# Optimization experiments

Hardware: AMD Instinct MI355X
Metric: run time of the kernel (lower is better)

The kernel has to match this reference:

```python
import jax, jax.numpy as jnp
import numpy as np

N_NODES = 100000
N_EDGES = 400000   # number of hyperedges
N_INC = 1600000    # incidence pairs (node, hyperedge)
N_GRAPHS = 512
ATOM_DIM = 92
NODE_DIM = 64
H_DIM = 128
NUM_LAYERS = 3
BN_EPS = 1e-5


def setup_inputs() -> dict:
    key = jax.random.key(0)
    ks = jax.random.split(key, 10)
    x = jax.random.normal(ks[0], (N_NODES, ATOM_DIM), jnp.float32)
    node_idx = jax.random.randint(ks[1], (N_INC,), 0, N_NODES)
    edge_idx = jax.random.randint(ks[2], (N_INC,), 0, N_EDGES)
    batch = jnp.sort(jax.random.randint(ks[3], (N_NODES,), 0, N_GRAPHS))

    def lin(k, fan_in, shape):
        return jax.random.normal(k, shape, jnp.float32) / np.float32(np.sqrt(fan_in))

    W_emb = lin(ks[4], ATOM_DIM, (ATOM_DIM, NODE_DIM))
    b_emb = jnp.zeros((NODE_DIM,), jnp.float32)
    conv_W = lin(ks[5], NODE_DIM, (NUM_LAYERS, NODE_DIM, NODE_DIM))
    conv_b = jnp.zeros((NUM_LAYERS, NODE_DIM), jnp.float32)
    bn_gamma = jnp.ones((NUM_LAYERS, NODE_DIM), jnp.float32)
    bn_beta = jnp.zeros((NUM_LAYERS, NODE_DIM), jnp.float32)
    fc_W = lin(ks[6], NODE_DIM, (NODE_DIM, H_DIM))
    fc_b = jnp.zeros((H_DIM,), jnp.float32)
    fco_W = lin(ks[7], H_DIM, (H_DIM, 1))
    fco_b = jnp.zeros((1,), jnp.float32)
    return {
        "x": x, "W_emb": W_emb, "b_emb": b_emb,
        "conv_W": conv_W, "conv_b": conv_b,
        "bn_gamma": bn_gamma, "bn_beta": bn_beta,
        "fc_W": fc_W, "fc_b": fc_b, "fco_W": fco_W, "fco_b": fco_b,
        "node_idx": node_idx, "edge_idx": edge_idx, "batch": batch,
    }


def _hypergraph_conv(h, W, b, gamma, beta, node_idx, edge_idx):
    """PyG-style HypergraphConv: X' = D^-1 H B^-1 H^T (X Theta), then BN + softplus."""
    h = h @ W + b  # [N, F]
    ones = jnp.ones((N_INC,), h.dtype)
    deg_e = jax.ops.segment_sum(ones, edge_idx, num_segments=N_EDGES)  # |e| per hyperedge
    Binv = jnp.where(deg_e > 0, 1.0 / deg_e, 0.0)
    # node -> hyperedge: mean of member node features
    e_feat = jax.ops.segment_sum(h[node_idx], edge_idx, num_segments=N_EDGES) * Binv[:, None]
    deg_n = jax.ops.segment_sum(ones, node_idx, num_segments=N_NODES)  # node hyperedge-degree
    Dinv = jnp.where(deg_n > 0, 1.0 / deg_n, 0.0)
    # hyperedge -> node
    out = jax.ops.segment_sum(e_feat[edge_idx], node_idx, num_segments=N_NODES) * Dinv[:, None]
    # BatchNorm1d over node dimension (training-mode batch statistics, biased var)
    mean = out.mean(axis=0)
    var = jnp.mean(jnp.square(out - mean), axis=0)
    out = gamma * (out - mean) * jax.lax.rsqrt(var + BN_EPS) + beta
    return jax.nn.softplus(out)


def reference(x, W_emb, b_emb, conv_W, conv_b, bn_gamma, bn_beta,
              fc_W, fc_b, fco_W, fco_b, node_idx, edge_idx, batch):
    h = x @ W_emb + b_emb  # [N, node_dim]
    for l in range(NUM_LAYERS):
        h = _hypergraph_conv(h, conv_W[l], conv_b[l], bn_gamma[l], bn_beta[l],
                             node_idx, edge_idx)
    # scatter-mean pooling over graphs
    cnt = jax.ops.segment_sum(jnp.ones((N_NODES,), h.dtype), batch, num_segments=N_GRAPHS)
    pooled = jax.ops.segment_sum(h, batch, num_segments=N_GRAPHS) / jnp.maximum(cnt, 1.0)[:, None]
    g = jax.nn.softplus(pooled)
    g = jax.nn.softplus(g @ fc_W + fc_b)
    return g @ fco_W + fco_b  # [N_GRAPHS, 1]
```

## Files before the change

kernel.cpp:

```cpp
#include <hip/hip_runtime.h>
#include <hip/hip_fp16.h>
#include <math.h>

#define N_NODES   100000
#define N_EDGES   400000
#define N_INC     1600000
#define N_GRAPHS  512
#define ATOM_DIM  92
#define NODE_DIM  64
#define H_DIM     128
#define NUM_LAYERS 3
#define BN_EPS    1e-5f

#define NBUCK     391
#define PCHUNK    2048
#define NCHP      ((N_INC + PCHUNK - 1) / PCHUNK)
#define MM_BLOCKS 1568

struct alignas(8)  half4 { __half2 a, b; };
struct alignas(16) half8 { __half2 a, b, c, d; };
typedef __attribute__((ext_vector_type(8))) float float8;
typedef __attribute__((ext_vector_type(2))) float float2v;
typedef __attribute__((ext_vector_type(4))) float f32x4;
typedef _Float16 f16x8 __attribute__((ext_vector_type(8)));

__device__ __forceinline__ float softplus_f(float x) {
    return fmaxf(x, 0.f) + log1pf(expf(-fabsf(x)));
}

__device__ __forceinline__ float8 cvt8(half8 v) {
    float2 p0 = __half22float2(v.a), p1 = __half22float2(v.b);
    float2 p2 = __half22float2(v.c), p3 = __half22float2(v.d);
    float8 r;
    r[0] = p0.x; r[1] = p0.y; r[2] = p1.x; r[3] = p1.y;
    r[4] = p2.x; r[5] = p2.y; r[6] = p3.x; r[7] = p3.y;
    return r;
}
__device__ __forceinline__ half8 cvt16(float8 v) {
    half8 r;
    r.a = __floats2half2_rn(v[0], v[1]);
    r.b = __floats2half2_rn(v[2], v[3]);
    r.c = __floats2half2_rn(v[4], v[5]);
    r.d = __floats2half2_rn(v[6], v[7]);
    return r;
}

__device__ __forceinline__ float8 fp8x8_to_f32u(unsigned lo, unsigned hi) {
    float2v l0 = __builtin_amdgcn_cvt_pk_f32_fp8((int)lo, false);
    float2v h0 = __builtin_amdgcn_cvt_pk_f32_fp8((int)lo, true);
    float2v l1 = __builtin_amdgcn_cvt_pk_f32_fp8((int)hi, false);
    float2v h1 = __builtin_amdgcn_cvt_pk_f32_fp8((int)hi, true);
    float8 r;
    r[0] = l0.x; r[1] = l0.y; r[2] = h0.x; r[3] = h0.y;
    r[4] = l1.x; r[5] = l1.y; r[6] = h1.x; r[7] = h1.y;
    return r;
}
__device__ __forceinline__ float8 fp8x8_to_f32(uint2 v) {
    return fp8x8_to_f32u(v.x, v.y);
}
__device__ __forceinline__ uint2 f32_to_fp8x8(float8 v) {
    int a = 0, b = 0;
    a = __builtin_amdgcn_cvt_pk_fp8_f32(v[0], v[1], a, false);
    a = __builtin_amdgcn_cvt_pk_fp8_f32(v[2], v[3], a, true);
    b = __builtin_amdgcn_cvt_pk_fp8_f32(v[4], v[5], b, false);
    b = __builtin_amdgcn_cvt_pk_fp8_f32(v[6], v[7], b, true);
    uint2 r; r.x = (unsigned)a; r.y = (unsigned)b;
    return r;
}


__global__ void __launch_bounds__(256) embed_mfma(
        const float* __restrict__ x, const float* __restrict__ W,
        const float* __restrict__ bvec, uint2* __restrict__ h8) {
    __shared__ half8 so8[4][16][9];
    int tid = threadIdx.x;
    int w = tid >> 6, lane = tid & 63;
    int l15 = lane & 15, rg = lane >> 4;
    __half* so_h = (__half*)so8[w];

    f16x8 bf[4][3];
    #pragma unroll
    for (int c = 0; c < 4; ++c)
        #pragma unroll
        for (int kk = 0; kk < 3; ++kk)
            #pragma unroll
            for (int j = 0; j < 8; ++j) {
                int k = kk * 32 + rg * 8 + j;
                bf[c][kk][j] = (k < ATOM_DIM) ? (_Float16)W[k * 64 + c * 16 + l15]
                                              : (_Float16)0.f;
            }
    float bias[4];
    #pragma unroll
    for (int c = 0; c < 4; ++c) bias[c] = bvec[c * 16 + l15];

    int wave_global = blockIdx.x * 4 + w;
    for (int tile = wave_global; tile < N_NODES / 16; tile += MM_BLOCKS * 4) {
        int n0 = tile * 16;
        const float* xrow = x + (size_t)(n0 + l15) * ATOM_DIM;
        f16x8 af[3];
        #pragma unroll
        for (int kk = 0; kk < 3; ++kk) {
            int k0 = kk * 32 + rg * 8;
            if (k0 + 8 <= ATOM_DIM) {
                float4 v0 = *(const float4*)&xrow[k0];
                float4 v1 = *(const float4*)&xrow[k0 + 4];
                af[kk][0] = (_Float16)v0.x; af[kk][1] = (_Float16)v0.y;
                af[kk][2] = (_Float16)v0.z; af[kk][3] = (_Float16)v0.w;
                af[kk][4] = (_Float16)v1.x; af[kk][5] = (_Float16)v1.y;
                af[kk][6] = (_Float16)v1.z; af[kk][7] = (_Float16)v1.w;
            } else {
                float4 v0 = *(const float4*)&xrow[88];
                af[kk][0] = (_Float16)v0.x; af[kk][1] = (_Float16)v0.y;
                af[kk][2] = (_Float16)v0.z; af[kk][3] = (_Float16)v0.w;
                af[kk][4] = (_Float16)0.f;  af[kk][5] = (_Float16)0.f;
                af[kk][6] = (_Float16)0.f;  af[kk][7] = (_Float16)0.f;
            }
        }
        #pragma unroll
        for (int c = 0; c < 4; ++c) {
            f32x4 acc = {0.f, 0.f, 0.f, 0.f};
            acc = __builtin_amdgcn_mfma_f32_16x16x32_f16(af[0], bf[c][0], acc, 0, 0, 0);
            acc = __builtin_amdgcn_mfma_f32_16x16x32_f16(af[1], bf[c][1], acc, 0, 0, 0);
            acc = __builtin_amdgcn_mfma_f32_16x16x32_f16(af[2], bf[c][2], acc, 0, 0, 0);
            #pragma unroll
            for (int i = 0; i < 4; ++i)
                so_h[(rg * 4 + i) * 72 + c * 16 + l15] = __float2half_rn(acc[i] + bias[c]);
        }
        #pragma unroll
        for (int it = 0; it < 2; ++it) {
            int row = (lane >> 3) + it * 8;
            half8 v = *(half8*)&so_h[row * 72 + (lane & 7) * 8];
            h8[(size_t)(n0 + row) * 8 + (lane & 7)] = f32_to_fp8x8(cvt8(v));
        }
    }
}


__global__ void __launch_bounds__(256) part_hist_dual(
        const int* __restrict__ ekey, const int* __restrict__ nkey,
        int* __restrict__ histsE, int* __restrict__ histsN) {
    __shared__ int hE[NBUCK];
    __shared__ int hN[NBUCK];
    int tid = threadIdx.x;
    int base = blockIdx.x * PCHUNK;
    for (int i = tid; i < NBUCK; i += 256) { hE[i] = 0; hN[i] = 0; }
    __syncthreads();
    #pragma unroll
    for (int k = 0; k < 8; ++k) {
        int i = base + tid + k * 256;
        if (i < N_INC) {
            atomicAdd(&hE[ekey[i] >> 10], 1);
            atomicAdd(&hN[nkey[i] >> 8], 1);
        }
    }
    __syncthreads();
    for (int i = tid; i < NBUCK; i += 256) {
        histsE[(size_t)blockIdx.x * NBUCK + i] = hE[i];
        histsN[(size_t)blockIdx.x * NBUCK + i] = hN[i];
    }
}

__global__ void __launch_bounds__(256) col_scan_dual(
        int* __restrict__ histsE, int* __restrict__ histsN,
        int* __restrict__ colsumE, int* __restrict__ colsumN) {
    __shared__ int ws[256];
    int which = blockIdx.x >= NBUCK;
    int i = which ? (blockIdx.x - NBUCK) : blockIdx.x;
    int* hists = which ? histsN : histsE;
    int* colsum = which ? colsumN : colsumE;
    int tid = threadIdx.x;
    int v[4];
    int loc = 0;
    #pragma unroll
    for (int k = 0; k < 4; ++k) {
        int b = tid * 4 + k;
        v[k] = (b < NCHP) ? hists[(size_t)b * NBUCK + i] : 0;
        loc += v[k];
    }
    ws[tid] = loc;
    __syncthreads();
    for (int off = 1; off < 256; off <<= 1) {
        int t = (tid >= off) ? ws[tid - off] : 0;
        __syncthreads();
        ws[tid] += t;
        __syncthreads();
    }
    int run = ws[tid] - loc;
    if (tid == 255) colsum[i] = ws[255];
    #pragma unroll
    for (int k = 0; k < 4; ++k) {
        int b = tid * 4 + k;
        if (b < NCHP) hists[(size_t)b * NBUCK + i] = run;
        run += v[k];
    }
}

__global__ void bbase_scan_dual(const int* __restrict__ colsumE, const int* __restrict__ colsumN,
                                int* __restrict__ bbaseE, int* __restrict__ bbaseN) {
    __shared__ int sh[512];
    const int* colsum = blockIdx.x ? colsumN : colsumE;
    int* bbase = blockIdx.x ? bbaseN : bbaseE;
    int tid = threadIdx.x;
    int v = (tid < NBUCK) ? colsum[tid] : 0;
    sh[tid] = v;
    __syncthreads();
    for (int off = 1; off < 512; off <<= 1) {
        int t = (tid >= off) ? sh[tid - off] : 0;
        __syncthreads();
        sh[tid] += t;
        __syncthreads();
    }
    if (tid <= NBUCK)
        bbase[tid] = (tid == 0) ? 0 : sh[tid - 1];
}

__global__ void __launch_bounds__(256) part_scatter_dual(
        const int* __restrict__ ekey, const int* __restrict__ nkey,
        const int* __restrict__ histsE, const int* __restrict__ histsN,
        const int* __restrict__ bbaseE, const int* __restrict__ bbaseN,
        unsigned long long* __restrict__ stagingE,
        unsigned long long* __restrict__ stagingN) {
    __shared__ int curE[NBUCK];
    __shared__ int curN[NBUCK];
    int tid = threadIdx.x;
    int base = blockIdx.x * PCHUNK;
    int kE[8], kN[8];
    #pragma unroll
    for (int k = 0; k < 8; ++k) {
        int i = base + tid + k * 256;
        bool ok = (i < N_INC);
        kE[k] = ok ? ekey[i] : -1;
        kN[k] = ok ? nkey[i] : 0;
    }
    for (int i = tid; i < NBUCK; i += 256) {
        curE[i] = bbaseE[i] + histsE[(size_t)blockIdx.x * NBUCK + i];
        curN[i] = bbaseN[i] + histsN[(size_t)blockIdx.x * NBUCK + i];
    }
    __syncthreads();
    #pragma unroll
    for (int k = 0; k < 8; ++k) {
        if (kE[k] >= 0) {
            int pe = atomicAdd(&curE[kE[k] >> 10], 1);
            stagingE[pe] = ((unsigned long long)(unsigned)kE[k] << 32) | (unsigned)kN[k];
            int pn = atomicAdd(&curN[kN[k] >> 8], 1);
            stagingN[pn] = ((unsigned long long)(unsigned)kN[k] << 32) | (unsigned)kE[k];
        }
    }
}

template<int RANGE>
__global__ void bucket_finalize(const unsigned long long* __restrict__ staging,
                                const int* __restrict__ bbase,
                                int nIds, float* __restrict__ inv,
                                int* __restrict__ off, int* __restrict__ list) {
    __shared__ int hist[RANGE];
    __shared__ int wsum[256];
    const int PER = RANGE / 256;
    int b = blockIdx.x, tid = threadIdx.x;
    int s = bbase[b], t = bbase[b + 1];
    int id0 = b * RANGE;
    for (int i = tid; i < RANGE; i += 256) hist[i] = 0;
    __syncthreads();
    for (int j = s + tid; j < t; j += 256) {
        int key = (int)(staging[j] >> 32);
        atomicAdd(&hist[key - id0], 1);
    }
    __syncthreads();
    int base0 = tid * PER;
    int vals[PER];
    int local = 0;
    #pragma unroll
    for (int k = 0; k < PER; ++k) { vals[k] = hist[base0 + k]; local += vals[k]; }
    wsum[tid] = local;
    __syncthreads();
    for (int o = 1; o < 256; o <<= 1) {
        int tv = (tid >= o) ? wsum[tid - o] : 0;
        __syncthreads();
        wsum[tid] += tv;
        __syncthreads();
    }
    int run = wsum[tid] - local;
    #pragma unroll
    for (int k = 0; k < PER; ++k) {
        int id = id0 + base0 + k;
        int gpos = s + run;
        if (id < nIds) {
            off[id] = gpos;
            inv[id] = vals[k] > 0 ? 1.f / (float)vals[k] : 0.f;
        } else if (id == nIds) {
            off[nIds] = gpos;
        }
        hist[base0 + k] = gpos;
        run += vals[k];
    }
    __syncthreads();
    for (int j = s + tid; j < t; j += 256) {
        unsigned long long it = staging[j];
        int key = (int)(it >> 32);
        int pos = atomicAdd(&hist[key - id0], 1);
        list[pos] = (int)(it & 0xffffffffu);
    }
}


__global__ void __launch_bounds__(256) edge_agg(
        const int* __restrict__ eoff, const int* __restrict__ elist,
        const uint4* __restrict__ h16B, const float* __restrict__ binv,
        uint4* __restrict__ efeat16B) {
    int e = blockIdx.x * 64 + (threadIdx.x >> 2);
    if (e >= N_EDGES) return;
    int q = threadIdx.x & 3;
    int s = eoff[e], t = eoff[e + 1];
    float8 alo = (float8)0.f, ahi = (float8)0.f;
    float8 blo = (float8)0.f, bhi = (float8)0.f;
    int j = s;
    for (; j + 1 < t; j += 2) {
        int n0 = __ldg(&elist[j]), n1 = __ldg(&elist[j + 1]);
        uint4 v0 = __ldg(&h16B[(size_t)n0 * 4 + q]);
        uint4 v1 = __ldg(&h16B[(size_t)n1 * 4 + q]);
        alo += fp8x8_to_f32u(v0.x, v0.y); ahi += fp8x8_to_f32u(v0.z, v0.w);
        blo += fp8x8_to_f32u(v1.x, v1.y); bhi += fp8x8_to_f32u(v1.z, v1.w);
    }
    if (j < t) {
        uint4 v0 = __ldg(&h16B[(size_t)__ldg(&elist[j]) * 4 + q]);
        alo += fp8x8_to_f32u(v0.x, v0.y); ahi += fp8x8_to_f32u(v0.z, v0.w);
    }
    alo += blo; ahi += bhi;
    float bv = binv[e];
    alo *= bv; ahi *= bv;
    uint2 lo = f32_to_fp8x8(alo), hi = f32_to_fp8x8(ahi);
    uint4 st; st.x = lo.x; st.y = lo.y; st.z = hi.x; st.w = hi.y;
    efeat16B[(size_t)e * 4 + q] = st;
}

__global__ void __launch_bounds__(256) node_agg(
        const int* __restrict__ noff, const int* __restrict__ nlist,
        const uint4* __restrict__ efeat16B, const float* __restrict__ dinv,
        __half* __restrict__ agg16) {
    int n = blockIdx.x * 64 + (threadIdx.x >> 2);
    if (n >= N_NODES) return;
    int q = threadIdx.x & 3;
    int s = noff[n], t = noff[n + 1];
    float8 alo = (float8)0.f, ahi = (float8)0.f;
    float8 blo = (float8)0.f, bhi = (float8)0.f;
    int j = s;
    for (; j + 1 < t; j += 2) {
        int e0 = __ldg(&nlist[j]), e1 = __ldg(&nlist[j + 1]);
        uint4 v0 = __ldg(&efeat16B[(size_t)e0 * 4 + q]);
        uint4 v1 = __ldg(&efeat16B[(size_t)e1 * 4 + q]);
        alo += fp8x8_to_f32u(v0.x, v0.y); ahi += fp8x8_to_f32u(v0.z, v0.w);
        blo += fp8x8_to_f32u(v1.x, v1.y); bhi += fp8x8_to_f32u(v1.z, v1.w);
    }
    if (j < t) {
        uint4 v0 = __ldg(&efeat16B[(size_t)__ldg(&nlist[j]) * 4 + q]);
        alo += fp8x8_to_f32u(v0.x, v0.y); ahi += fp8x8_to_f32u(v0.z, v0.w);
    }
    alo += blo; ahi += bhi;
    float dv = dinv[n];
    alo *= dv; ahi *= dv;
    *(half8*)&agg16[(size_t)n * 64 + q * 16]     = cvt16(alo);
    *(half8*)&agg16[(size_t)n * 64 + q * 16 + 8] = cvt16(ahi);
}


__global__ void __launch_bounds__(256) gemm_bn_kernel(
        const __half* __restrict__ agg16, const float* __restrict__ dinv,
        const float* __restrict__ W, const float* __restrict__ bvec,
        __half* __restrict__ outr16, float* __restrict__ partials) {
    __shared__ half8 so8[4][16][9];
    __shared__ float sred[4][128];
    int tid = threadIdx.x;
    int w = tid >> 6, lane = tid & 63;
    int l15 = lane & 15, rg = lane >> 4;
    __half* so_h = (__half*)so8[w];

    f16x8 bf[4][2];
    #pragma unroll
    for (int c = 0; c < 4; ++c)
        #pragma unroll
        for (int kk = 0; kk < 2; ++kk)
            #pragma unroll
            for (int j = 0; j < 8; ++j) {
                int k = kk * 32 + rg * 8 + j;
                bf[c][kk][j] = (_Float16)W[k * 64 + c * 16 + l15];
            }
    float bias[4];
    #pragma unroll
    for (int c = 0; c < 4; ++c) bias[c] = bvec[c * 16 + l15];

    float sa[4] = {0.f, 0.f, 0.f, 0.f}, sb[4] = {0.f, 0.f, 0.f, 0.f};
    int wave_global = blockIdx.x * 4 + w;
    for (int tile = wave_global; tile < N_NODES / 16; tile += MM_BLOCKS * 4) {
        int n0 = tile * 16;
        f16x8 a0 = *(const f16x8*)&agg16[(size_t)(n0 + l15) * 64 + rg * 8];
        f16x8 a1 = *(const f16x8*)&agg16[(size_t)(n0 + l15) * 64 + 32 + rg * 8];
        float dv[4];
        #pragma unroll
        for (int i = 0; i < 4; ++i) dv[i] = dinv[n0 + rg * 4 + i];
        #pragma unroll
        for (int c = 0; c < 4; ++c) {
            f32x4 acc = {0.f, 0.f, 0.f, 0.f};
            acc = __builtin_amdgcn_mfma_f32_16x16x32_f16(a0, bf[c][0], acc, 0, 0, 0);
            acc = __builtin_amdgcn_mfma_f32_16x16x32_f16(a1, bf[c][1], acc, 0, 0, 0);
            #pragma unroll
            for (int i = 0; i < 4; ++i) {
                float vv = (dv[i] > 0.f) ? (acc[i] + bias[c]) : 0.f;
                sa[c] += vv; sb[c] += vv * vv;
                so_h[(rg * 4 + i) * 72 + c * 16 + l15] = __float2half_rn(vv);
            }
        }
        #pragma unroll
        for (int it = 0; it < 2; ++it) {
            int row = (lane >> 3) + it * 8;
            half8 v = *(half8*)&so_h[row * 72 + (lane & 7) * 8];
            *(half8*)&outr16[(size_t)(n0 + row) * 64 + (lane & 7) * 8] = v;
        }
    }
    #pragma unroll
    for (int c = 0; c < 4; ++c) {
        sa[c] += __shfl_xor(sa[c], 16); sa[c] += __shfl_xor(sa[c], 32);
        sb[c] += __shfl_xor(sb[c], 16); sb[c] += __shfl_xor(sb[c], 32);
    }
    if (rg == 0) {
        #pragma unroll
        for (int c = 0; c < 4; ++c) {
            sred[w][c * 16 + l15]      = sa[c];
            sred[w][64 + c * 16 + l15] = sb[c];
        }
    }
    __syncthreads();
    if (tid < 128) {
        float v = sred[0][tid] + sred[1][tid] + sred[2][tid] + sred[3][tid];
        partials[(size_t)blockIdx.x * 128 + tid] = v;
    }
}


__global__ void __launch_bounds__(256) reduce_bnfin(
        const float* __restrict__ partials, const float* __restrict__ gamma,
        const float* __restrict__ beta, float* __restrict__ scsh) {
    __shared__ float ra[256];
    __shared__ float rb[256];
    int f = blockIdx.x, tid = threadIdx.x;
    float a = 0.f, b = 0.f;
    for (int j = tid; j < MM_BLOCKS; j += 256) {
        a += partials[(size_t)j * 128 + f];
        b += partials[(size_t)j * 128 + 64 + f];
    }
    ra[tid] = a; rb[tid] = b;
    __syncthreads();
    for (int s = 128; s > 0; s >>= 1) {
        if (tid < s) { ra[tid] += ra[tid + s]; rb[tid] += rb[tid + s]; }
        __syncthreads();
    }
    if (tid == 0) {
        const float invN = 1.f / (float)N_NODES;
        float mean = ra[0] * invN;
        float var  = rb[0] * invN - mean * mean;
        var = fmaxf(var, 0.f);
        float sc = gamma[f] * rsqrtf(var + BN_EPS);
        scsh[f]      = sc;
        scsh[64 + f] = beta[f] - mean * sc;
    }
}


__global__ void apply_kernel(const half8* __restrict__ outr8, const float* __restrict__ scsh,
                             uint2* __restrict__ h8) {
    int gid = blockIdx.x * 256 + threadIdx.x;
    if (gid >= N_NODES * 8) return;
    int qq = gid & 7;
    float8 v = cvt8(outr8[gid]);
    float4 sc0 = ((const float4*)scsh)[qq * 2];
    float4 sc1 = ((const float4*)scsh)[qq * 2 + 1];
    float4 sh0 = ((const float4*)(scsh + 64))[qq * 2];
    float4 sh1 = ((const float4*)(scsh + 64))[qq * 2 + 1];
    float8 r;
    r[0] = softplus_f(fmaf(v[0], sc0.x, sh0.x));
    r[1] = softplus_f(fmaf(v[1], sc0.y, sh0.y));
    r[2] = softplus_f(fmaf(v[2], sc0.z, sh0.z));
    r[3] = softplus_f(fmaf(v[3], sc0.w, sh0.w));
    r[4] = softplus_f(fmaf(v[4], sc1.x, sh1.x));
    r[5] = softplus_f(fmaf(v[5], sc1.y, sh1.y));
    r[6] = softplus_f(fmaf(v[6], sc1.z, sh1.z));
    r[7] = softplus_f(fmaf(v[7], sc1.w, sh1.w));
    h8[gid] = f32_to_fp8x8(r);
}


__global__ void graph_bounds(const int* __restrict__ batch, int* __restrict__ goff) {
    int g = blockIdx.x * 256 + threadIdx.x;
    if (g > N_GRAPHS) return;
    int lo = 0, hi = N_NODES;
    while (lo < hi) {
        int mid = (lo + hi) >> 1;
        if (batch[mid] < g) lo = mid + 1; else hi = mid;
    }
    goff[g] = lo;
}

__global__ void pool_head_kernel(const uint2* __restrict__ h8, const int* __restrict__ goff,
                                 const float* __restrict__ fcW, const float* __restrict__ fcb,
                                 const float* __restrict__ fcoW, const float* __restrict__ fcob,
                                 float* __restrict__ out) {
    __shared__ float8 part[32][8];
    __shared__ float p[64];
    __shared__ float red[128];
    int g = blockIdx.x, tid = threadIdx.x;
    int s = goff[g], t = goff[g + 1];
    int r = tid >> 3, q = tid & 7;
    float8 acc = (float8)0.f;
    for (int n = s + r; n < t; n += 32)
        acc += fp8x8_to_f32(__ldg(&h8[(size_t)n * 8 + q]));
    part[r][q] = acc;
    __syncthreads();
    for (int st = 16; st >= 1; st >>= 1) {
        if (r < st) part[r][q] += part[r + st][q];
        __syncthreads();
    }
    if (tid < 8) {
        float c = fmaxf((float)(t - s), 1.f);
        float8 v = part[0][tid];
        #pragma unroll
        for (int jj = 0; jj < 8; ++jj)
            p[tid * 8 + jj] = softplus_f(v[jj] / c);
    }
    __syncthreads();
    if (tid < 128) {
        float a = fcb[tid];
        #pragma unroll
        for (int k = 0; k < 64; ++k)
            a = fmaf(p[k], fcW[k * H_DIM + tid], a);
        red[tid] = softplus_f(a) * fcoW[tid];
    }
    __syncthreads();
    for (int st = 64; st > 0; st >>= 1) {
        if (tid < st) red[tid] += red[tid + st];
        __syncthreads();
    }
    if (tid == 0) out[g] = red[0] + fcob[0];
}


extern "C" void kernel_launch(void* const* d_in, const int* in_sizes, int n_in,
                              void* d_out, int out_size, void* d_ws, size_t ws_size,
                              hipStream_t stream) {
    const float* x      = (const float*)d_in[0];
    const float* W_emb  = (const float*)d_in[1];
    const float* b_emb  = (const float*)d_in[2];
    const float* conv_W = (const float*)d_in[3];
    const float* conv_b = (const float*)d_in[4];
    const float* bn_g   = (const float*)d_in[5];
    const float* bn_b   = (const float*)d_in[6];
    const float* fc_W   = (const float*)d_in[7];
    const float* fc_b   = (const float*)d_in[8];
    const float* fco_W  = (const float*)d_in[9];
    const float* fco_b  = (const float*)d_in[10];
    const int* node_idx = (const int*)d_in[11];
    const int* edge_idx = (const int*)d_in[12];
    const int* batch    = (const int*)d_in[13];
    float* out = (float*)d_out;

    uint2*  h8      = (uint2*)d_ws;
    __half* outr16  = (__half*)(h8 + (size_t)N_NODES * 8);
    __half* agg16   = outr16 + (size_t)N_NODES * 64;
    uint2*  efeat8  = (uint2*)(agg16 + (size_t)N_NODES * 64);
    unsigned long long* stagingE = (unsigned long long*)(efeat8 + (size_t)N_EDGES * 8);
    unsigned long long* stagingN = stagingE + N_INC;
    float* binv    = (float*)(stagingN + N_INC);
    float* dinv    = binv   + N_EDGES;
    float* scsh    = dinv   + N_NODES;
    float* partials= scsh   + 128;
    int*   goff    = (int*)(partials + (size_t)MM_BLOCKS * 128);
    int*   eoff    = goff  + N_GRAPHS + 1;
    int*   noff    = eoff  + N_EDGES + 1;
    int*   histsE  = noff  + N_NODES + 1;
    int*   histsN  = histsE + (size_t)NCHP * NBUCK;
    int*   colsumE = histsN + (size_t)NCHP * NBUCK;
    int*   colsumN = colsumE + NBUCK;
    int*   bbaseE  = colsumN + NBUCK;
    int*   bbaseN  = bbaseE + NBUCK + 1;
    int*   elist   = bbaseN + NBUCK + 1;
    int*   nlist   = elist + N_INC;

    part_hist_dual<<<NCHP, 256, 0, stream>>>(edge_idx, node_idx, histsE, histsN);
    col_scan_dual<<<2 * NBUCK, 256, 0, stream>>>(histsE, histsN, colsumE, colsumN);
    bbase_scan_dual<<<2, 512, 0, stream>>>(colsumE, colsumN, bbaseE, bbaseN);
    part_scatter_dual<<<NCHP, 256, 0, stream>>>(edge_idx, node_idx, histsE, histsN,
                                                bbaseE, bbaseN, stagingE, stagingN);
    bucket_finalize<1024><<<NBUCK, 256, 0, stream>>>(stagingE, bbaseE, N_EDGES, binv, eoff, elist);
    bucket_finalize<256><<<NBUCK, 256, 0, stream>>>(stagingN, bbaseN, N_NODES, dinv, noff, nlist);

    graph_bounds<<<(N_GRAPHS + 1 + 255) / 256, 256, 0, stream>>>(batch, goff);

    embed_mfma<<<MM_BLOCKS, 256, 0, stream>>>(x, W_emb, b_emb, h8);

    for (int l = 0; l < NUM_LAYERS; ++l) {
        const float* Wl = conv_W + (size_t)l * NODE_DIM * NODE_DIM;
        const float* bl = conv_b + (size_t)l * NODE_DIM;

        edge_agg<<<(N_EDGES + 63) / 64, 256, 0, stream>>>(eoff, elist, (const uint4*)h8,
                                                          binv, (uint4*)efeat8);
        node_agg<<<(N_NODES + 63) / 64, 256, 0, stream>>>(noff, nlist, (const uint4*)efeat8,
                                                          dinv, agg16);
        gemm_bn_kernel<<<MM_BLOCKS, 256, 0, stream>>>(agg16, dinv, Wl, bl, outr16, partials);
        reduce_bnfin<<<64, 256, 0, stream>>>(partials, bn_g + (size_t)l * 64,
                                             bn_b + (size_t)l * 64, scsh);
        apply_kernel<<<(N_NODES * 8 + 255) / 256, 256, 0, stream>>>((const half8*)outr16, scsh, h8);
    }

    pool_head_kernel<<<N_GRAPHS, 256, 0, stream>>>(h8, goff, fc_W, fc_b, fco_W, fco_b, out);
}
```

Before: 408.8 us.

## Pack staging to 32-bit, merge finalize kernels, unroll node_agg, inline graph bounds

Staging entries go from 64-bit to 32-bit by storing only the key offset within its bucket plus the payload. This halves the scatter and finalize traffic. The two bucket_finalize launches become one dual-role kernel, and the graph_bounds kernel is folded into pool_head as a per-block binary search, which removes launches. node_agg now unrolls 4-way with more independent accumulators so more gathers are in flight.

```diff
diff --git a/kernel.cpp b/kernel.cpp
--- a/kernel.cpp
+++ b/kernel.cpp
@@ -218,8 +218,7 @@
         const int* __restrict__ ekey, const int* __restrict__ nkey,
         const int* __restrict__ histsE, const int* __restrict__ histsN,
         const int* __restrict__ bbaseE, const int* __restrict__ bbaseN,
-        unsigned long long* __restrict__ stagingE,
-        unsigned long long* __restrict__ stagingN) {
+        unsigned* __restrict__ stagingE, unsigned* __restrict__ stagingN) {
     __shared__ int curE[NBUCK];
     __shared__ int curN[NBUCK];
     int tid = threadIdx.x;
@@ -241,29 +240,29 @@
     for (int k = 0; k < 8; ++k) {
         if (kE[k] >= 0) {
             int pe = atomicAdd(&curE[kE[k] >> 10], 1);
-            stagingE[pe] = ((unsigned long long)(unsigned)kE[k] << 32) | (unsigned)kN[k];
+            stagingE[pe] = ((unsigned)(kE[k] & 1023) << 17) | (unsigned)kN[k];
             int pn = atomicAdd(&curN[kN[k] >> 8], 1);
-            stagingN[pn] = ((unsigned long long)(unsigned)kN[k] << 32) | (unsigned)kE[k];
-        }
-    }
-}
-
-template<int RANGE>
-__global__ void bucket_finalize(const unsigned long long* __restrict__ staging,
-                                const int* __restrict__ bbase,
-                                int nIds, float* __restrict__ inv,
-                                int* __restrict__ off, int* __restrict__ list) {
-    __shared__ int hist[RANGE];
-    __shared__ int wsum[256];
+            stagingN[pn] = ((unsigned)(kN[k] & 255) << 19) | (unsigned)kE[k];
+        }
+    }
+}
+
+template<int RANGE, int PAYBITS>
+__device__ void finalize_impl(const unsigned* __restrict__ staging,
+                              const int* __restrict__ bbase, int b,
+                              int nIds, float* __restrict__ inv,
+                              int* __restrict__ off, int* __restrict__ list,
+                              int* hist, int* wsum) {
     const int PER = RANGE / 256;
-    int b = blockIdx.x, tid = threadIdx.x;
+    const unsigned PAYMASK = (1u << PAYBITS) - 1u;
+    int tid = threadIdx.x;
     int s = bbase[b], t = bbase[b + 1];
     int id0 = b * RANGE;
     for (int i = tid; i < RANGE; i += 256) hist[i] = 0;
     __syncthreads();
     for (int j = s + tid; j < t; j += 256) {
-        int key = (int)(staging[j] >> 32);
-        atomicAdd(&hist[key - id0], 1);
+        unsigned key = staging[j] >> PAYBITS;
+        atomicAdd(&hist[key], 1);
     }
     __syncthreads();
     int base0 = tid * PER;
@@ -295,10 +294,27 @@
     }
     __syncthreads();
     for (int j = s + tid; j < t; j += 256) {
-        unsigned long long it = staging[j];
-        int key = (int)(it >> 32);
-        int pos = atomicAdd(&hist[key - id0], 1);
-        list[pos] = (int)(it & 0xffffffffu);
+        unsigned it = staging[j];
+        unsigned key = it >> PAYBITS;
+        int pos = atomicAdd(&hist[key], 1);
+        list[pos] = (int)(it & PAYMASK);
+    }
+}
+
+__global__ void __launch_bounds__(256) bucket_finalize_dual(
+        const unsigned* __restrict__ stagingE, const unsigned* __restrict__ stagingN,
+        const int* __restrict__ bbaseE, const int* __restrict__ bbaseN,
+        float* __restrict__ binv, float* __restrict__ dinv,
+        int* __restrict__ eoff, int* __restrict__ noff,
+        int* __restrict__ elist, int* __restrict__ nlist) {
+    __shared__ int hist[1024];
+    __shared__ int wsum[256];
+    if (blockIdx.x < NBUCK) {
+        finalize_impl<1024, 17>(stagingE, bbaseE, blockIdx.x, N_EDGES, binv, eoff, elist,
+                                hist, wsum);
+    } else {
+        finalize_impl<256, 19>(stagingN, bbaseN, blockIdx.x - NBUCK, N_NODES, dinv, noff, nlist,
+                               hist, wsum);
     }
 }
 
@@ -341,25 +357,33 @@
     if (n >= N_NODES) return;
     int q = threadIdx.x & 3;
     int s = noff[n], t = noff[n + 1];
-    float8 alo = (float8)0.f, ahi = (float8)0.f;
-    float8 blo = (float8)0.f, bhi = (float8)0.f;
+    float8 l0 = (float8)0.f, h0 = (float8)0.f;
+    float8 l1 = (float8)0.f, h1 = (float8)0.f;
+    float8 l2 = (float8)0.f, h2 = (float8)0.f;
+    float8 l3 = (float8)0.f, h3 = (float8)0.f;
     int j = s;
-    for (; j + 1 < t; j += 2) {
-        int e0 = __ldg(&nlist[j]), e1 = __ldg(&nlist[j + 1]);
+    for (; j + 3 < t; j += 4) {
+        int e0 = __ldg(&nlist[j]),     e1 = __ldg(&nlist[j + 1]);
+        int e2 = __ldg(&nlist[j + 2]), e3 = __ldg(&nlist[j + 3]);
         uint4 v0 = __ldg(&efeat16B[(size_t)e0 * 4 + q]);
         uint4 v1 = __ldg(&efeat16B[(size_t)e1 * 4 + q]);
-        alo += fp8x8_to_f32u(v0.x, v0.y); ahi += fp8x8_to_f32u(v0.z, v0.w);
-        blo += fp8x8_to_f32u(v1.x, v1.y); bhi += fp8x8_to_f32u(v1.z, v1.w);
-    }
-    if (j < t) {
+        uint4 v2 = __ldg(&efeat16B[(size_t)e2 * 4 + q]);
+        uint4 v3 = __ldg(&efeat16B[(size_t)e3 * 4 + q]);
+        l0 += fp8x8_to_f32u(v0.x, v0.y); h0 += fp8x8_to_f32u(v0.z, v0.w);
+        l1 += fp8x8_to_f32u(v1.x, v1.y); h1 += fp8x8_to_f32u(v1.z, v1.w);
+        l2 += fp8x8_to_f32u(v2.x, v2.y); h2 += fp8x8_to_f32u(v2.z, v2.w);
+        l3 += fp8x8_to_f32u(v3.x, v3.y); h3 += fp8x8_to_f32u(v3.z, v3.w);
+    }
+    for (; j < t; ++j) {
         uint4 v0 = __ldg(&efeat16B[(size_t)__ldg(&nlist[j]) * 4 + q]);
-        alo += fp8x8_to_f32u(v0.x, v0.y); ahi += fp8x8_to_f32u(v0.z, v0.w);
-    }
-    alo += blo; ahi += bhi;
+        l0 += fp8x8_to_f32u(v0.x, v0.y); h0 += fp8x8_to_f32u(v0.z, v0.w);
+    }
+    l0 += l1; l2 += l3; l0 += l2;
+    h0 += h1; h2 += h3; h0 += h2;
     float dv = dinv[n];
-    alo *= dv; ahi *= dv;
-    *(half8*)&agg16[(size_t)n * 64 + q * 16]     = cvt16(alo);
-    *(half8*)&agg16[(size_t)n * 64 + q * 16 + 8] = cvt16(ahi);
+    l0 *= dv; h0 *= dv;
+    *(half8*)&agg16[(size_t)n * 64 + q * 16]     = cvt16(l0);
+    *(half8*)&agg16[(size_t)n * 64 + q * 16 + 8] = cvt16(h0);
 }
 
 
@@ -488,26 +512,26 @@
 }
 
 
-__global__ void graph_bounds(const int* __restrict__ batch, int* __restrict__ goff) {
-    int g = blockIdx.x * 256 + threadIdx.x;
-    if (g > N_GRAPHS) return;
-    int lo = 0, hi = N_NODES;
-    while (lo < hi) {
-        int mid = (lo + hi) >> 1;
-        if (batch[mid] < g) lo = mid + 1; else hi = mid;
-    }
-    goff[g] = lo;
-}
-
-__global__ void pool_head_kernel(const uint2* __restrict__ h8, const int* __restrict__ goff,
+__global__ void pool_head_kernel(const uint2* __restrict__ h8, const int* __restrict__ batch,
                                  const float* __restrict__ fcW, const float* __restrict__ fcb,
                                  const float* __restrict__ fcoW, const float* __restrict__ fcob,
                                  float* __restrict__ out) {
     __shared__ float8 part[32][8];
     __shared__ float p[64];
     __shared__ float red[128];
+    __shared__ int seg[2];
     int g = blockIdx.x, tid = threadIdx.x;
-    int s = goff[g], t = goff[g + 1];
+    if (tid < 2) {
+        int target = g + tid;
+        int lo = 0, hi = N_NODES;
+        while (lo < hi) {
+            int mid = (lo + hi) >> 1;
+            if (batch[mid] < target) lo = mid + 1; else hi = mid;
+        }
+        seg[tid] = lo;
+    }
+    __syncthreads();
+    int s = seg[0], t = seg[1];
     int r = tid >> 3, q = tid & 7;
     float8 acc = (float8)0.f;
     for (int n = s + r; n < t; n += 32)
@@ -565,14 +589,13 @@
     __half* outr16  = (__half*)(h8 + (size_t)N_NODES * 8);
     __half* agg16   = outr16 + (size_t)N_NODES * 64;
     uint2*  efeat8  = (uint2*)(agg16 + (size_t)N_NODES * 64);
-    unsigned long long* stagingE = (unsigned long long*)(efeat8 + (size_t)N_EDGES * 8);
-    unsigned long long* stagingN = stagingE + N_INC;
+    unsigned* stagingE = (unsigned*)(efeat8 + (size_t)N_EDGES * 8);
+    unsigned* stagingN = stagingE + N_INC;
     float* binv    = (float*)(stagingN + N_INC);
     float* dinv    = binv   + N_EDGES;
     float* scsh    = dinv   + N_NODES;
     float* partials= scsh   + 128;
-    int*   goff    = (int*)(partials + (size_t)MM_BLOCKS * 128);
-    int*   eoff    = goff  + N_GRAPHS + 1;
+    int*   eoff    = (int*)(partials + (size_t)MM_BLOCKS * 128);
     int*   noff    = eoff  + N_EDGES + 1;
     int*   histsE  = noff  + N_NODES + 1;
     int*   histsN  = histsE + (size_t)NCHP * NBUCK;
@@ -588,10 +611,8 @@
     bbase_scan_dual<<<2, 512, 0, stream>>>(colsumE, colsumN, bbaseE, bbaseN);
     part_scatter_dual<<<NCHP, 256, 0, stream>>>(edge_idx, node_idx, histsE, histsN,
                                                 bbaseE, bbaseN, stagingE, stagingN);
-    bucket_finalize<1024><<<NBUCK, 256, 0, stream>>>(stagingE, bbaseE, N_EDGES, binv, eoff, elist);
-    bucket_finalize<256><<<NBUCK, 256, 0, stream>>>(stagingN, bbaseN, N_NODES, dinv, noff, nlist);
-
-    graph_bounds<<<(N_GRAPHS + 1 + 255) / 256, 256, 0, stream>>>(batch, goff);
+    bucket_finalize_dual<<<2 * NBUCK, 256, 0, stream>>>(stagingE, stagingN, bbaseE, bbaseN,
+                                                        binv, dinv, eoff, noff, elist, nlist);
 
     embed_mfma<<<MM_BLOCKS, 256, 0, stream>>>(x, W_emb, b_emb, h8);
 
@@ -609,5 +630,5 @@
         apply_kernel<<<(N_NODES * 8 + 255) / 256, 256, 0, stream>>>((const half8*)outr16, scsh, h8);
     }
 
-    pool_head_kernel<<<N_GRAPHS, 256, 0, stream>>>(h8, goff, fc_W, fc_b, fco_W, fco_b, out);
-}
+    pool_head_kernel<<<N_GRAPHS, 256, 0, stream>>>(h8, batch, fc_W, fc_b, fco_W, fco_b, out);
+}
```

Result: no change. 410.5 us (+0.4%).
